# Performance work log

Hardware: AMD Instinct MI355X
Metric: run time of the kernel (lower is better)

Reference implementation:

```python
import jax, jax.numpy as jnp
import numpy as np

B_SZ, L, H, P = 16, 1024, 256, 256
DT_MIN, DT_MAX = 1e-3, 1e-1


def setup_inputs() -> dict:
    key = jax.random.key(0)
    ks = jax.random.split(key, 6)
    u = jax.random.normal(ks[0], (B_SZ, L, H), dtype=jnp.float32)
    # Stable diagonal init (stands in for HiPPO-LegS diag: negative real part,
    # spread imaginary parts) so exp(Lambda*Delta) has |.|<1 over long scans.
    Lambda_re = -0.5 * jnp.ones((P,), jnp.float32)
    Lambda_im = jnp.pi * jnp.arange(P, dtype=jnp.float32)
    Bp = jax.random.normal(ks[1], (P, H, 2), jnp.float32) / jnp.sqrt(2.0 * H)  # (P,H,2) real/imag
    Cp = jax.random.normal(ks[2], (H, P, 2), jnp.float32) / jnp.sqrt(2.0 * P)  # (H,P,2) real/imag
    D = jax.random.normal(ks[3], (H,), jnp.float32)
    log_step = (jax.random.uniform(ks[4], (P, 1), jnp.float32)
                * (jnp.log(DT_MAX) - jnp.log(DT_MIN)) + jnp.log(DT_MIN))
    return {"u": u, "Lambda_re": Lambda_re, "Lambda_im": Lambda_im,
            "B": Bp, "C": Cp, "D": D, "log_step": log_step}


def _binop(ei, ej):
    # S5 associative scan element: (A, Bu); compose linear recurrences.
    ai, bi = ei
    aj, bj = ej
    return aj * ai, aj * bi + bj


def reference(u, Lambda_re, Lambda_im, B, C, D, log_step):
    # clip_eigs=False, step_rescale=1.0, conj_sym=True, discretization='zoh'
    Lambda = Lambda_re + 1j * Lambda_im                     # (P,) complex
    B_tilde = B[..., 0] + 1j * B[..., 1]                    # (P,H) complex
    C_tilde = C[..., 0] + 1j * C[..., 1]                    # (H,P) complex
    Delta = jnp.exp(log_step[:, 0])                         # (P,)
    # ZOH discretization
    Lambda_bar = jnp.exp(Lambda * Delta)                    # (P,)
    B_bar = ((Lambda_bar - 1.0) / Lambda)[:, None] * B_tilde  # (P,H)
    # Input projection: (B, L, P) complex
    Bu = jnp.einsum('ph,blh->blp', B_bar, u.astype(B_bar.dtype))
    Lam = jnp.broadcast_to(Lambda_bar, Bu.shape)            # (B, L, P)
    # Parallel associative scan over time axis
    _, xs = jax.lax.associative_scan(_binop, (Lam, Bu), axis=1)  # states (B,L,P)
    # Output projection; conj_sym -> 2 * real part
    ys = 2.0 * jnp.einsum('hp,blp->blh', C_tilde, xs).real  # (B,L,H)
    return ys + D * u                                       # feedthrough
```

## Files before the change

kernel.cpp:

```cpp
#include <hip/hip_runtime.h>
#include <hip/hip_bf16.h>
#include <math.h>

#define BB     16
#define LSEQ   1024
#define HH     256
#define PP     256
#define LC     32
#define NC     (LSEQ/LC)
#define NCHUNK (BB*NC)

#define OFF_W1T  0u
#define OFF_W2T  262144u
#define OFF_PW   524288u
#define OFF_CEND 655360u
#define OFF_BAR  2752512u

typedef __attribute__((ext_vector_type(8))) short short8;
typedef __attribute__((ext_vector_type(4))) float floatx4;
typedef unsigned long long ull;

__device__ __forceinline__ float bf2f(unsigned hs) {
    union { unsigned u; float f; } v; v.u = hs << 16; return v.f;
}
__device__ __forceinline__ unsigned short f2bs(float f) {
    __hip_bfloat16 h = __float2bfloat16(f);
    union { __hip_bfloat16 h; unsigned short s; } v; v.h = h; return v.s;
}
__device__ __forceinline__ unsigned packbf(float r, float i) {
    return (unsigned)f2bs(r) | ((unsigned)f2bs(i) << 16);
}
__device__ __forceinline__ void async16(const void* g, void* l) {
    __builtin_amdgcn_global_load_lds(
        (const __attribute__((address_space(1))) unsigned*)g,
        (__attribute__((address_space(3))) unsigned*)l, 16, 0, 0);
}
__device__ __forceinline__ float2 lam_pow(float lr, float li, float dtt) {
    float m = expf(lr * dtt);
    return make_float2(m * cosf(li * dtt), m * sinf(li * dtt));
}
__device__ __forceinline__ void cohst64(ull* p, float2 v) {
    ull b; __builtin_memcpy(&b, &v, 8);
    __hip_atomic_store(p, b, __ATOMIC_RELAXED, __HIP_MEMORY_SCOPE_AGENT);
}

__device__ __forceinline__ void batchbar(char* base) {
    asm volatile("s_waitcnt vmcnt(0)" ::: "memory");
    __syncthreads();
    if (threadIdx.x == 0) {
        const unsigned b = blockIdx.x >> 5;
        unsigned* cnt  = (unsigned*)(base + b * 64);
        unsigned* flag = (unsigned*)(base + 2048 + b * 64);
        if (__hip_atomic_fetch_add(cnt, 1u, __ATOMIC_RELAXED,
                                   __HIP_MEMORY_SCOPE_AGENT) == 31u) {
            __hip_atomic_store(flag, 1u, __ATOMIC_RELAXED, __HIP_MEMORY_SCOPE_AGENT);
        } else {
            for (int it = 0; it < (1 << 18); ++it) {
                if (__hip_atomic_load(flag, __ATOMIC_RELAXED, __HIP_MEMORY_SCOPE_AGENT))
                    break;
                __builtin_amdgcn_s_sleep(2);
            }
        }
    }
    __syncthreads();
}

__global__ void k_prep(const float* __restrict__ Bm, const float* __restrict__ Cm,
                       const float* __restrict__ Lr, const float* __restrict__ Li,
                       const float* __restrict__ ls, char* __restrict__ ws) {
    int blk = blockIdx.x, t = threadIdx.x;
    if (blk < 256) {
        if (t < 128) {
            int p = blk;
            float lr = Lr[p], li = Li[p];
            float dt = expf(ls[p]);
            float2 lam = lam_pow(lr, li, dt);
            float den = lr * lr + li * li;
            float nr = lam.x - 1.0f, ni = lam.y;
            float cr = (nr * lr + ni * li) / den;
            float ci = (ni * lr - nr * li) / den;
            float4 bv = *(const float4*)(Bm + (size_t)p * 512 + 4 * t);
            unsigned* w1u = (unsigned*)(ws + OFF_W1T);
            w1u[(2 * p) * 128 + t]     = packbf(cr * bv.x - ci * bv.y, cr * bv.z - ci * bv.w);
            w1u[(2 * p + 1) * 128 + t] = packbf(cr * bv.y + ci * bv.x, cr * bv.w + ci * bv.z);
            if (t <= 32)
                ((float2*)(ws + OFF_PW))[t * 256 + p] = lam_pow(lr, li, dt * (float)t);
        }
        if (blk == 0)
            ((float4*)(ws + OFF_BAR))[t] = make_float4(0.f, 0.f, 0.f, 0.f);
    } else {
        int h = blk - 256, p = t;
        float c_r = Cm[(h * PP + p) * 2 + 0];
        float c_i = Cm[(h * PP + p) * 2 + 1];
        ((unsigned*)(ws + OFF_W2T))[h * 256 + p] = packbf(2.0f * c_r, -2.0f * c_i);
    }
}

#define XSTRS 520
#define XSTRD 260
#define CARR_OFF 33280
#define B1_OFF  16384
#define B2_OFF  35328

__global__ __launch_bounds__(512, 4) void k_main(
        const float* __restrict__ u, const float* __restrict__ Lr,
        const float* __restrict__ Li, const float* __restrict__ ls,
        const float* __restrict__ D, float* __restrict__ out,
        char* __restrict__ ws) {
    extern __shared__ char smem[];
    const int tid = threadIdx.x, bc = blockIdx.x;
    const int wave = tid >> 6, lane = tid & 63;
    const int q = lane >> 4, rr = lane & 15;
    const int m0 = bc * LC;
    const int fs = (lane >> 3) & 3;
    const int fr = (rr >> 1) & 3;

    {
        const char* W1 = (const char*)(ws + OFF_W1T);
        char* dst = smem + B1_OFF + wave * 4096;
        #pragma unroll
        for (int i = 0; i < 4; ++i) {
            int n = i * 64 + lane;
            int R = wave * 64 + (n >> 2);
            async16(W1 + (size_t)R * 512 + (((n & 3) ^ fs) << 4), dst + n * 16);
        }
    }

    const int arow = tid >> 4, acol = (tid & 15) * 16;
    {
        float4 uv[4];
        const float* up = u + (size_t)(m0 + arow) * 256 + acol;
        #pragma unroll
        for (int i = 0; i < 4; ++i) uv[i] = *(const float4*)(up + 4 * i);
        unsigned pk[8];
        #pragma unroll
        for (int i = 0; i < 4; ++i) {
            pk[2 * i]     = packbf(uv[i].x, uv[i].y);
            pk[2 * i + 1] = packbf(uv[i].z, uv[i].w);
        }
        const int kb = acol * 2;
        const int msk = (arow & 7) << 4;
        char* A = smem;
        *(uint4*)(A + arow * 512 + (kb ^ msk))        = make_uint4(pk[0], pk[1], pk[2], pk[3]);
        *(uint4*)(A + arow * 512 + ((kb + 16) ^ msk)) = make_uint4(pk[4], pk[5], pk[6], pk[7]);
    }
    __syncthreads();

    {
        const char* W1 = (const char*)(ws + OFF_W1T);
        const char* A = smem;
        const int amask = (rr & 7) << 4;
        floatx4 acc[2][4];
        #pragma unroll
        for (int i = 0; i < 2; ++i)
            #pragma unroll
            for (int j = 0; j < 4; ++j) acc[i][j] = (floatx4)0.0f;

        for (int t = 0; t < 8; ++t) {
            asm volatile("s_waitcnt vmcnt(0)" ::: "memory");
            if (t < 7) {
                char* dst = smem + B1_OFF + ((t + 1) & 1) * 32768 + wave * 4096;
                const char* src = W1 + (t + 1) * 64;
                #pragma unroll
                for (int i = 0; i < 4; ++i) {
                    int n = i * 64 + lane;
                    int R = wave * 64 + (n >> 2);
                    async16(src + (size_t)R * 512 + (((n & 3) ^ fs) << 4), dst + n * 16);
                }
            }
            const char* bb = smem + B1_OFF + (t & 1) * 32768 + wave * 4096;
            const int kbA = t * 64 + q * 16;
            short8 a0 = *(const short8*)(A + rr * 512 + (kbA ^ amask));
            short8 a1 = *(const short8*)(A + (16 + rr) * 512 + (kbA ^ amask));
            #pragma unroll
            for (int j = 0; j < 4; ++j) {
                short8 b = *(const short8*)(bb + (j * 16 + rr) * 64 + ((q ^ fr) << 4));
                acc[0][j] = __builtin_amdgcn_mfma_f32_16x16x32_bf16(a0, b, acc[0][j], 0, 0, 0);
                acc[1][j] = __builtin_amdgcn_mfma_f32_16x16x32_bf16(a1, b, acc[1][j], 0, 0, 0);
            }
        }
        __syncthreads();
        unsigned short* X = (unsigned short*)smem;
        #pragma unroll
        for (int i = 0; i < 2; ++i)
            #pragma unroll
            for (int j = 0; j < 4; ++j)
                #pragma unroll
                for (int r0 = 0; r0 < 4; ++r0)
                    X[(i * 16 + q * 4 + r0) * XSTRS + wave * 64 + j * 16 + rr] =
                        f2bs(acc[i][j][r0]);
        __syncthreads();
    }

    if (tid < 256) {
        const int pq = tid;
        const float2 lam = lam_pow(Lr[pq], Li[pq], expf(ls[pq]));
        unsigned* X32 = (unsigned*)smem;
        float xr = 0.0f, xi = 0.0f;
        #pragma unroll
        for (int j = 0; j < LC; ++j) {
            unsigned cv = X32[j * XSTRD + pq];
            float br = bf2f(cv & 0xffffu), bi = bf2f(cv >> 16);
            float nr = fmaf(lam.x, xr, fmaf(-lam.y, xi, br));
            float ni = fmaf(lam.x, xi, fmaf(lam.y, xr, bi));
            xr = nr; xi = ni;
            X32[j * XSTRD + pq] = packbf(xr, xi);
        }
        cohst64((ull*)(ws + OFF_CEND) + (size_t)bc * 256 + pq, make_float2(xr, xi));
    } else {
        const char* W2 = (const char*)(ws + OFF_W2T);
        char* B2 = smem + B2_OFF;
        const int t4 = tid - 256;
        const int f0 = (t4 >> 3) & 3;
        #pragma unroll
        for (int i = 0; i < 4; ++i) {
            int c = i * 256 + t4;
            int R = c >> 2;
            async16(W2 + (size_t)R * 1024 + (((c & 3) ^ f0) << 4), B2 + c * 16);
        }
    }
    batchbar(ws + OFF_BAR);

    {
        float2* carrs = (float2*)(smem + CARR_OFF);
        if (tid < 256) {
            const int p = tid;
            const int c = bc & (NC - 1);
            const int b0 = bc & ~(NC - 1);
            const float2* cend = (const float2*)(ws + OFF_CEND);
            const float2 g = lam_pow(Lr[p], Li[p], expf(ls[p]) * (float)LC);
            float sr = 0.0f, si = 0.0f;
            float gpr = 1.0f, gpi = 0.0f;
            #pragma unroll
            for (int k = 0; k < NC - 1; ++k) {
                int idx = c - 1 - k; idx = idx < 0 ? 0 : idx;
                float2 e = cend[(size_t)(b0 + idx) * 256 + p];
                float er = (k < c) ? e.x : 0.0f;
                float ei = (k < c) ? e.y : 0.0f;
                sr = fmaf(gpr, er, fmaf(-gpi, ei, sr));
                si = fmaf(gpr, ei, fmaf(gpi, er, si));
                float t2 = gpr * g.x - gpi * g.y;
                gpi = gpr * g.y + gpi * g.x; gpr = t2;
            }
            carrs[p] = make_float2(sr, si);
        }
        __syncthreads();
    }

    {
        float2* carrs = (float2*)(smem + CARR_OFF);
        unsigned* X32 = (unsigned*)smem;
        const float2* pw = (const float2*)(ws + OFF_PW);
        const int frow = tid >> 4, fcol = tid & 15;
        const float2* pwr = pw + (size_t)(frow + 1) * 256;
        #pragma unroll 4
        for (int e = 0; e < 16; ++e) {
            int p = fcol + e * 16;
            unsigned cv = X32[frow * XSTRD + p];
            float2 pwv = pwr[p];
            float2 cav = carrs[p];
            float fr2 = pwv.x * cav.x - pwv.y * cav.y;
            float fi2 = pwv.x * cav.y + pwv.y * cav.x;
            X32[frow * XSTRD + p] =
                packbf(bf2f(cv & 0xffffu) + fr2, bf2f(cv >> 16) + fi2);
        }
        __syncthreads();
    }

    {
        const char* W2 = (const char*)(ws + OFF_W2T);
        const char* Xb = (const char*)smem;
        floatx4 acc[2][2];
        #pragma unroll
        for (int i = 0; i < 2; ++i)
            #pragma unroll
            for (int j = 0; j < 2; ++j) acc[i][j] = (floatx4)0.0f;

        for (int t = 0; t < 16; ++t) {
            asm volatile("s_waitcnt vmcnt(0)" ::: "memory");
            if (t < 15) {
                char* dst = smem + B2_OFF + ((t + 1) & 1) * 16384 + wave * 2048;
                const char* src = W2 + (t + 1) * 64;
                #pragma unroll
                for (int i = 0; i < 2; ++i) {
                    int n = i * 64 + lane;
                    int R = wave * 32 + (n >> 2);
                    async16(src + (size_t)R * 1024 + (((n & 3) ^ fs) << 4), dst + n * 16);
                }
            }
            const char* bbuf = smem + B2_OFF + (t & 1) * 16384 + wave * 2048;
            const int kbA = t * 64 + q * 16;
            short8 a0 = *(const short8*)(Xb + rr * (XSTRS * 2) + kbA);
            short8 a1 = *(const short8*)(Xb + (16 + rr) * (XSTRS * 2) + kbA);
            #pragma unroll
            for (int j = 0; j < 2; ++j) {
                short8 b = *(const short8*)(bbuf + (j * 16 + rr) * 64 + ((q ^ fr) << 4));
                acc[0][j] = __builtin_amdgcn_mfma_f32_16x16x32_bf16(a0, b, acc[0][j], 0, 0, 0);
                acc[1][j] = __builtin_amdgcn_mfma_f32_16x16x32_bf16(a1, b, acc[1][j], 0, 0, 0);
            }
        }

        #pragma unroll
        for (int i = 0; i < 2; ++i) {
            int mbase = m0 + i * 16 + q * 4;
            #pragma unroll
            for (int j = 0; j < 2; ++j) {
                int col = wave * 32 + j * 16 + rr;
                #pragma unroll
                for (int r0 = 0; r0 < 4; ++r0) {
                    int rw = mbase + r0;
                    size_t gi = (size_t)rw * 256 + col;
                    out[gi] = acc[i][j][r0] + D[col] * u[gi];
                }
            }
        }
    }
}

extern "C" void kernel_launch(void* const* d_in, const int* in_sizes, int n_in,
                              void* d_out, int out_size, void* d_ws, size_t ws_size,
                              hipStream_t stream) {
    const float* u  = (const float*)d_in[0];
    const float* Lr = (const float*)d_in[1];
    const float* Li = (const float*)d_in[2];
    const float* Bm = (const float*)d_in[3];
    const float* Cm = (const float*)d_in[4];
    const float* D  = (const float*)d_in[5];
    const float* ls = (const float*)d_in[6];
    float* out = (float*)d_out;
    char* ws = (char*)d_ws;

    k_prep<<<512, 256, 0, stream>>>(Bm, Cm, Lr, Li, ls, ws);
    k_main<<<NCHUNK, 512, 81920, stream>>>(u, Lr, Li, ls, D, out, ws);
}
```

Baseline: 104.0 us.

## Load MFMA weight fragments directly into registers with triple/quad buffering

Replaces the LDS-staged double-buffered async global-to-LDS copies of the W1 and W2 weight tiles with direct per-lane global loads into register slots. Loads are issued several k-steps ahead through a rotating 3-slot (W1) or 4-slot (W2) register pipeline, which removes the per-step vmcnt(0) waits and the LDS round trip. W2 prefetch now starts right after the batch barrier, so it overlaps the carry computation. LDS drops from 80 KB to about 35 KB, which allows more resident blocks, at the cost of more VGPRs and uncoalesced 16-byte global loads.

```diff
diff --git a/kernel.cpp b/kernel.cpp
--- a/kernel.cpp
+++ b/kernel.cpp
@@ -29,11 +29,6 @@
 }
 __device__ __forceinline__ unsigned packbf(float r, float i) {
     return (unsigned)f2bs(r) | ((unsigned)f2bs(i) << 16);
-}
-__device__ __forceinline__ void async16(const void* g, void* l) {
-    __builtin_amdgcn_global_load_lds(
-        (const __attribute__((address_space(1))) unsigned*)g,
-        (__attribute__((address_space(3))) unsigned*)l, 16, 0, 0);
 }
 __device__ __forceinline__ float2 lam_pow(float lr, float li, float dtt) {
     float m = expf(lr * dtt);
@@ -99,8 +94,8 @@
 #define XSTRS 520
 #define XSTRD 260
 #define CARR_OFF 33280
-#define B1_OFF  16384
-#define B2_OFF  35328
+
+#define MFMA16(a, b, c) __builtin_amdgcn_mfma_f32_16x16x32_bf16((a), (b), (c), 0, 0, 0)
 
 __global__ __launch_bounds__(512, 4) void k_main(
         const float* __restrict__ u, const float* __restrict__ Lr,
@@ -112,26 +107,25 @@
     const int wave = tid >> 6, lane = tid & 63;
     const int q = lane >> 4, rr = lane & 15;
     const int m0 = bc * LC;
-    const int fs = (lane >> 3) & 3;
-    const int fr = (rr >> 1) & 3;
-
-    {
-        const char* W1 = (const char*)(ws + OFF_W1T);
-        char* dst = smem + B1_OFF + wave * 4096;
-        #pragma unroll
-        for (int i = 0; i < 4; ++i) {
-            int n = i * 64 + lane;
-            int R = wave * 64 + (n >> 2);
-            async16(W1 + (size_t)R * 512 + (((n & 3) ^ fs) << 4), dst + n * 16);
-        }
-    }
 
     const int arow = tid >> 4, acol = (tid & 15) * 16;
-    {
-        float4 uv[4];
+    float4 uv[4];
+    {
         const float* up = u + (size_t)(m0 + arow) * 256 + acol;
         #pragma unroll
         for (int i = 0; i < 4; ++i) uv[i] = *(const float4*)(up + 4 * i);
+    }
+
+    const char* W1 = (const char*)(ws + OFF_W1T);
+    const char* W1w = W1 + (size_t)(wave * 64 + rr) * 512 + q * 16;
+    short8 b0[4], b1[4], b2[4];
+#define LOADB1(slot, t)                                              \
+    { _Pragma("unroll")                                              \
+      for (int j = 0; j < 4; ++j)                                    \
+          slot[j] = *(const short8*)(W1w + j * 8192 + (t) * 64); }
+    LOADB1(b0, 0) LOADB1(b1, 1) LOADB1(b2, 2)
+
+    {
         unsigned pk[8];
         #pragma unroll
         for (int i = 0; i < 4; ++i) {
@@ -147,7 +141,6 @@
     __syncthreads();
 
     {
-        const char* W1 = (const char*)(ws + OFF_W1T);
         const char* A = smem;
         const int amask = (rr & 7) << 4;
         floatx4 acc[2][4];
@@ -156,29 +149,25 @@
             #pragma unroll
             for (int j = 0; j < 4; ++j) acc[i][j] = (floatx4)0.0f;
 
-        for (int t = 0; t < 8; ++t) {
-            asm volatile("s_waitcnt vmcnt(0)" ::: "memory");
-            if (t < 7) {
-                char* dst = smem + B1_OFF + ((t + 1) & 1) * 32768 + wave * 4096;
-                const char* src = W1 + (t + 1) * 64;
-                #pragma unroll
-                for (int i = 0; i < 4; ++i) {
-                    int n = i * 64 + lane;
-                    int R = wave * 64 + (n >> 2);
-                    async16(src + (size_t)R * 512 + (((n & 3) ^ fs) << 4), dst + n * 16);
-                }
-            }
-            const char* bb = smem + B1_OFF + (t & 1) * 32768 + wave * 4096;
-            const int kbA = t * 64 + q * 16;
-            short8 a0 = *(const short8*)(A + rr * 512 + (kbA ^ amask));
-            short8 a1 = *(const short8*)(A + (16 + rr) * 512 + (kbA ^ amask));
-            #pragma unroll
-            for (int j = 0; j < 4; ++j) {
-                short8 b = *(const short8*)(bb + (j * 16 + rr) * 64 + ((q ^ fr) << 4));
-                acc[0][j] = __builtin_amdgcn_mfma_f32_16x16x32_bf16(a0, b, acc[0][j], 0, 0, 0);
-                acc[1][j] = __builtin_amdgcn_mfma_f32_16x16x32_bf16(a1, b, acc[1][j], 0, 0, 0);
-            }
-        }
+#define STEP1(t, slot)                                                        \
+    {   const int kbA = (t) * 64 + q * 16;                                    \
+        short8 a0 = *(const short8*)(A + rr * 512 + (kbA ^ amask));           \
+        short8 a1 = *(const short8*)(A + (16 + rr) * 512 + (kbA ^ amask));    \
+        _Pragma("unroll")                                                     \
+        for (int j = 0; j < 4; ++j) {                                         \
+            acc[0][j] = MFMA16(a0, slot[j], acc[0][j]);                       \
+            acc[1][j] = MFMA16(a1, slot[j], acc[1][j]);                       \
+        } }
+        STEP1(0, b0) LOADB1(b0, 3)
+        STEP1(1, b1) LOADB1(b1, 4)
+        STEP1(2, b2) LOADB1(b2, 5)
+        STEP1(3, b0) LOADB1(b0, 6)
+        STEP1(4, b1) LOADB1(b1, 7)
+        STEP1(5, b2)
+        STEP1(6, b0)
+        STEP1(7, b1)
+#undef STEP1
+#undef LOADB1
         __syncthreads();
         unsigned short* X = (unsigned short*)smem;
         #pragma unroll
@@ -207,26 +196,24 @@
             X32[j * XSTRD + pq] = packbf(xr, xi);
         }
         cohst64((ull*)(ws + OFF_CEND) + (size_t)bc * 256 + pq, make_float2(xr, xi));
-    } else {
-        const char* W2 = (const char*)(ws + OFF_W2T);
-        char* B2 = smem + B2_OFF;
-        const int t4 = tid - 256;
-        const int f0 = (t4 >> 3) & 3;
-        #pragma unroll
-        for (int i = 0; i < 4; ++i) {
-            int c = i * 256 + t4;
-            int R = c >> 2;
-            async16(W2 + (size_t)R * 1024 + (((c & 3) ^ f0) << 4), B2 + c * 16);
-        }
     }
     batchbar(ws + OFF_BAR);
+
+    const char* W2 = (const char*)(ws + OFF_W2T);
+    const char* W2w = W2 + (size_t)(wave * 32 + rr) * 1024 + q * 16;
+    short8 c0[2], c1[2], c2[2], c3[2];
+#define LOADB2(slot, t)                                              \
+    { _Pragma("unroll")                                              \
+      for (int j = 0; j < 2; ++j)                                    \
+          slot[j] = *(const short8*)(W2w + j * 16384 + (t) * 64); }
+    LOADB2(c0, 0) LOADB2(c1, 1) LOADB2(c2, 2) LOADB2(c3, 3)
 
     {
         float2* carrs = (float2*)(smem + CARR_OFF);
         if (tid < 256) {
             const int p = tid;
             const int c = bc & (NC - 1);
-            const int b0 = bc & ~(NC - 1);
+            const int b0i = bc & ~(NC - 1);
             const float2* cend = (const float2*)(ws + OFF_CEND);
             const float2 g = lam_pow(Lr[p], Li[p], expf(ls[p]) * (float)LC);
             float sr = 0.0f, si = 0.0f;
@@ -234,7 +221,7 @@
             #pragma unroll
             for (int k = 0; k < NC - 1; ++k) {
                 int idx = c - 1 - k; idx = idx < 0 ? 0 : idx;
-                float2 e = cend[(size_t)(b0 + idx) * 256 + p];
+                float2 e = cend[(size_t)(b0i + idx) * 256 + p];
                 float er = (k < c) ? e.x : 0.0f;
                 float ei = (k < c) ? e.y : 0.0f;
                 sr = fmaf(gpr, er, fmaf(-gpi, ei, sr));
@@ -268,7 +255,6 @@
     }
 
     {
-        const char* W2 = (const char*)(ws + OFF_W2T);
         const char* Xb = (const char*)smem;
         floatx4 acc[2][2];
         #pragma unroll
@@ -276,29 +262,33 @@
             #pragma unroll
             for (int j = 0; j < 2; ++j) acc[i][j] = (floatx4)0.0f;
 
-        for (int t = 0; t < 16; ++t) {
-            asm volatile("s_waitcnt vmcnt(0)" ::: "memory");
-            if (t < 15) {
-                char* dst = smem + B2_OFF + ((t + 1) & 1) * 16384 + wave * 2048;
-                const char* src = W2 + (t + 1) * 64;
-                #pragma unroll
-                for (int i = 0; i < 2; ++i) {
-                    int n = i * 64 + lane;
-                    int R = wave * 32 + (n >> 2);
-                    async16(src + (size_t)R * 1024 + (((n & 3) ^ fs) << 4), dst + n * 16);
-                }
-            }
-            const char* bbuf = smem + B2_OFF + (t & 1) * 16384 + wave * 2048;
-            const int kbA = t * 64 + q * 16;
-            short8 a0 = *(const short8*)(Xb + rr * (XSTRS * 2) + kbA);
-            short8 a1 = *(const short8*)(Xb + (16 + rr) * (XSTRS * 2) + kbA);
-            #pragma unroll
-            for (int j = 0; j < 2; ++j) {
-                short8 b = *(const short8*)(bbuf + (j * 16 + rr) * 64 + ((q ^ fr) << 4));
-                acc[0][j] = __builtin_amdgcn_mfma_f32_16x16x32_bf16(a0, b, acc[0][j], 0, 0, 0);
-                acc[1][j] = __builtin_amdgcn_mfma_f32_16x16x32_bf16(a1, b, acc[1][j], 0, 0, 0);
-            }
-        }
+#define STEP2(t, slot)                                                        \
+    {   const int kbA = (t) * 64 + q * 16;                                    \
+        short8 a0 = *(const short8*)(Xb + rr * (XSTRS * 2) + kbA);            \
+        short8 a1 = *(const short8*)(Xb + (16 + rr) * (XSTRS * 2) + kbA);     \
+        _Pragma("unroll")                                                     \
+        for (int j = 0; j < 2; ++j) {                                         \
+            acc[0][j] = MFMA16(a0, slot[j], acc[0][j]);                       \
+            acc[1][j] = MFMA16(a1, slot[j], acc[1][j]);                       \
+        } }
+        STEP2(0,  c0) LOADB2(c0, 4)
+        STEP2(1,  c1) LOADB2(c1, 5)
+        STEP2(2,  c2) LOADB2(c2, 6)
+        STEP2(3,  c3) LOADB2(c3, 7)
+        STEP2(4,  c0) LOADB2(c0, 8)
+        STEP2(5,  c1) LOADB2(c1, 9)
+        STEP2(6,  c2) LOADB2(c2, 10)
+        STEP2(7,  c3) LOADB2(c3, 11)
+        STEP2(8,  c0) LOADB2(c0, 12)
+        STEP2(9,  c1) LOADB2(c1, 13)
+        STEP2(10, c2) LOADB2(c2, 14)
+        STEP2(11, c3) LOADB2(c3, 15)
+        STEP2(12, c0)
+        STEP2(13, c1)
+        STEP2(14, c2)
+        STEP2(15, c3)
+#undef STEP2
+#undef LOADB2
 
         #pragma unroll
         for (int i = 0; i < 2; ++i) {
@@ -331,5 +321,5 @@
     char* ws = (char*)d_ws;
 
     k_prep<<<512, 256, 0, stream>>>(Bm, Cm, Lr, Li, ls, ws);
-    k_main<<<NCHUNK, 512, 81920, stream>>>(u, Lr, Li, ls, D, out, ws);
-}
+    k_main<<<NCHUNK, 512, 35328, stream>>>(u, Lr, Li, ls, D, out, ws);
+}
```

After: 117.6 us. +13.1%, slower.

## Deepen weight prefetch to two stages in both MFMA GEMM loops

Applied to the files above, without the earlier changes.

Both bf16 GEMM K-loops now keep two async weight-panel loads in flight. Before the scan barrier, the second panel of each GEMM is prefetched in addition to the first. Each iteration waits only for the oldest panel (vmcnt(4)/vmcnt(2)), copies the B fragments into registers, then starts the t+2 load into the buffer it just drained. The loops are fully unrolled with a sched_barrier so global latency can overlap the MFMAs instead of draining with vmcnt(0) every step. This adds register pressure, and correctness depends on the hand-counted vmcnt values and buffer reuse ordering.

```diff
diff --git a/kernel.cpp b/kernel.cpp
--- a/kernel.cpp
+++ b/kernel.cpp
@@ -115,8 +115,8 @@
     const int fs = (lane >> 3) & 3;
     const int fr = (rr >> 1) & 3;
 
-    {
-        const char* W1 = (const char*)(ws + OFF_W1T);
+    const char* W1 = (const char*)(ws + OFF_W1T);
+    {
         char* dst = smem + B1_OFF + wave * 4096;
         #pragma unroll
         for (int i = 0; i < 4; ++i) {
@@ -144,10 +144,20 @@
         *(uint4*)(A + arow * 512 + (kb ^ msk))        = make_uint4(pk[0], pk[1], pk[2], pk[3]);
         *(uint4*)(A + arow * 512 + ((kb + 16) ^ msk)) = make_uint4(pk[4], pk[5], pk[6], pk[7]);
     }
+
+    {
+        char* dst = smem + B1_OFF + 32768 + wave * 4096;
+        const char* src = W1 + 64;
+        #pragma unroll
+        for (int i = 0; i < 4; ++i) {
+            int n = i * 64 + lane;
+            int R = wave * 64 + (n >> 2);
+            async16(src + (size_t)R * 512 + (((n & 3) ^ fs) << 4), dst + n * 16);
+        }
+    }
     __syncthreads();
 
     {
-        const char* W1 = (const char*)(ws + OFF_W1T);
         const char* A = smem;
         const int amask = (rr & 7) << 4;
         floatx4 acc[2][4];
@@ -156,11 +166,23 @@
             #pragma unroll
             for (int j = 0; j < 4; ++j) acc[i][j] = (floatx4)0.0f;
 
+        #pragma unroll
         for (int t = 0; t < 8; ++t) {
-            asm volatile("s_waitcnt vmcnt(0)" ::: "memory");
-            if (t < 7) {
-                char* dst = smem + B1_OFF + ((t + 1) & 1) * 32768 + wave * 4096;
-                const char* src = W1 + (t + 1) * 64;
+            if (t < 7) { asm volatile("s_waitcnt vmcnt(4)" ::: "memory"); }
+            else       { asm volatile("s_waitcnt vmcnt(0)" ::: "memory"); }
+            const char* bb = smem + B1_OFF + (t & 1) * 32768 + wave * 4096;
+            const int kbA = t * 64 + q * 16;
+            short8 a0 = *(const short8*)(A + rr * 512 + (kbA ^ amask));
+            short8 a1 = *(const short8*)(A + (16 + rr) * 512 + (kbA ^ amask));
+            short8 bfr[4];
+            #pragma unroll
+            for (int j = 0; j < 4; ++j)
+                bfr[j] = *(const short8*)(bb + (j * 16 + rr) * 64 + ((q ^ fr) << 4));
+            asm volatile("s_waitcnt lgkmcnt(0)" ::: "memory");
+            __builtin_amdgcn_sched_barrier(0);
+            if (t < 6) {
+                char* dst = smem + B1_OFF + (t & 1) * 32768 + wave * 4096;
+                const char* src = W1 + (t + 2) * 64;
                 #pragma unroll
                 for (int i = 0; i < 4; ++i) {
                     int n = i * 64 + lane;
@@ -168,15 +190,10 @@
                     async16(src + (size_t)R * 512 + (((n & 3) ^ fs) << 4), dst + n * 16);
                 }
             }
-            const char* bb = smem + B1_OFF + (t & 1) * 32768 + wave * 4096;
-            const int kbA = t * 64 + q * 16;
-            short8 a0 = *(const short8*)(A + rr * 512 + (kbA ^ amask));
-            short8 a1 = *(const short8*)(A + (16 + rr) * 512 + (kbA ^ amask));
             #pragma unroll
             for (int j = 0; j < 4; ++j) {
-                short8 b = *(const short8*)(bb + (j * 16 + rr) * 64 + ((q ^ fr) << 4));
-                acc[0][j] = __builtin_amdgcn_mfma_f32_16x16x32_bf16(a0, b, acc[0][j], 0, 0, 0);
-                acc[1][j] = __builtin_amdgcn_mfma_f32_16x16x32_bf16(a1, b, acc[1][j], 0, 0, 0);
+                acc[0][j] = __builtin_amdgcn_mfma_f32_16x16x32_bf16(a0, bfr[j], acc[0][j], 0, 0, 0);
+                acc[1][j] = __builtin_amdgcn_mfma_f32_16x16x32_bf16(a1, bfr[j], acc[1][j], 0, 0, 0);
             }
         }
         __syncthreads();
@@ -213,10 +230,14 @@
         const int t4 = tid - 256;
         const int f0 = (t4 >> 3) & 3;
         #pragma unroll
-        for (int i = 0; i < 4; ++i) {
-            int c = i * 256 + t4;
-            int R = c >> 2;
-            async16(W2 + (size_t)R * 1024 + (((c & 3) ^ f0) << 4), B2 + c * 16);
+        for (int pan = 0; pan < 2; ++pan) {
+            #pragma unroll
+            for (int i = 0; i < 4; ++i) {
+                int c = i * 256 + t4;
+                int R = c >> 2;
+                async16(W2 + (size_t)R * 1024 + pan * 64 + (((c & 3) ^ f0) << 4),
+                        B2 + pan * 16384 + c * 16);
+            }
         }
     }
     batchbar(ws + OFF_BAR);
@@ -276,11 +297,23 @@
             #pragma unroll
             for (int j = 0; j < 2; ++j) acc[i][j] = (floatx4)0.0f;
 
+        #pragma unroll
         for (int t = 0; t < 16; ++t) {
-            asm volatile("s_waitcnt vmcnt(0)" ::: "memory");
-            if (t < 15) {
-                char* dst = smem + B2_OFF + ((t + 1) & 1) * 16384 + wave * 2048;
-                const char* src = W2 + (t + 1) * 64;
+            if (t < 15) { asm volatile("s_waitcnt vmcnt(2)" ::: "memory"); }
+            else        { asm volatile("s_waitcnt vmcnt(0)" ::: "memory"); }
+            const char* bbuf = smem + B2_OFF + (t & 1) * 16384 + wave * 2048;
+            const int kbA = t * 64 + q * 16;
+            short8 a0 = *(const short8*)(Xb + rr * (XSTRS * 2) + kbA);
+            short8 a1 = *(const short8*)(Xb + (16 + rr) * (XSTRS * 2) + kbA);
+            short8 bfr[2];
+            #pragma unroll
+            for (int j = 0; j < 2; ++j)
+                bfr[j] = *(const short8*)(bbuf + (j * 16 + rr) * 64 + ((q ^ fr) << 4));
+            asm volatile("s_waitcnt lgkmcnt(0)" ::: "memory");
+            __builtin_amdgcn_sched_barrier(0);
+            if (t < 14) {
+                char* dst = smem + B2_OFF + (t & 1) * 16384 + wave * 2048;
+                const char* src = W2 + (t + 2) * 64;
                 #pragma unroll
                 for (int i = 0; i < 2; ++i) {
                     int n = i * 64 + lane;
@@ -288,15 +321,10 @@
                     async16(src + (size_t)R * 1024 + (((n & 3) ^ fs) << 4), dst + n * 16);
                 }
             }
-            const char* bbuf = smem + B2_OFF + (t & 1) * 16384 + wave * 2048;
-            const int kbA = t * 64 + q * 16;
-            short8 a0 = *(const short8*)(Xb + rr * (XSTRS * 2) + kbA);
-            short8 a1 = *(const short8*)(Xb + (16 + rr) * (XSTRS * 2) + kbA);
             #pragma unroll
             for (int j = 0; j < 2; ++j) {
-                short8 b = *(const short8*)(bbuf + (j * 16 + rr) * 64 + ((q ^ fr) << 4));
-                acc[0][j] = __builtin_amdgcn_mfma_f32_16x16x32_bf16(a0, b, acc[0][j], 0, 0, 0);
-                acc[1][j] = __builtin_amdgcn_mfma_f32_16x16x32_bf16(a1, b, acc[1][j], 0, 0, 0);
+                acc[0][j] = __builtin_amdgcn_mfma_f32_16x16x32_bf16(a0, bfr[j], acc[0][j], 0, 0, 0);
+                acc[1][j] = __builtin_amdgcn_mfma_f32_16x16x32_bf16(a1, bfr[j], acc[1][j], 0, 0, 0);
             }
         }
 
```

After: 104.1 us. No clear change (+0.1%).
